# Optimization experiments

Hardware: AMD Instinct MI355X
Metric: run time of the kernel (lower is better)

Reference implementation:

```python
import jax, jax.numpy as jnp
import numpy as np

N_NODES = 50000
N_EDGES = 1600000
N_GRAPHS = 64
DIMS = [3, 256, 256, 256]  # in -> hidden -> hidden -> output
BN_EPS = 1e-5


def setup_inputs() -> dict:
    key = jax.random.key(0)
    ks = jax.random.split(key, 32)
    inp = {}
    inp['x'] = jax.random.normal(ks[0], (N_NODES, DIMS[0]), dtype=jnp.float32)
    inp['edge_index'] = jax.random.randint(ks[1], (2, N_EDGES), 0, N_NODES, dtype=jnp.int64)
    inp['batch'] = jnp.sort(jax.random.randint(ks[2], (N_NODES,), 0, N_GRAPHS, dtype=jnp.int64))
    k = 3
    for i in range(3):
        fi, fo = DIMS[i], DIMS[i + 1]
        inp[f'W{i}'] = jax.random.normal(ks[k], (fi, fo), dtype=jnp.float32) / np.sqrt(fi); k += 1
        inp[f'b{i}'] = jnp.zeros((fo,), dtype=jnp.float32)
        inp[f'g{i}'] = jnp.ones((fo,), dtype=jnp.float32)       # BN weight
        inp[f'be{i}'] = jnp.zeros((fo,), dtype=jnp.float32)     # BN bias
        inp[f'm{i}'] = 0.1 * jax.random.normal(ks[k], (fo,), dtype=jnp.float32); k += 1  # running mean
        inp[f'v{i}'] = jax.random.uniform(ks[k], (fo,), dtype=jnp.float32) + 0.5; k += 1  # running var
    return inp


def _gcn_norm(edge_index, n_nodes):
    # add self-loops, compute symmetric normalization (PyG GCNConv gcn_norm)
    loops = jnp.arange(n_nodes, dtype=edge_index.dtype)
    src = jnp.concatenate([edge_index[0], loops])
    dst = jnp.concatenate([edge_index[1], loops])
    deg = jax.ops.segment_sum(jnp.ones_like(dst, dtype=jnp.float32), dst, num_segments=n_nodes)
    dinv = jnp.where(deg > 0, jax.lax.rsqrt(deg), 0.0)
    norm = dinv[src] * dinv[dst]  # [E+N]
    return src, dst, norm


def _gcn_conv(x, W, b, src, dst, norm, n_nodes):
    h = x @ W                                 # [N, out]
    msg = h[src] * norm[:, None]              # gather + edge weight
    out = jax.ops.segment_sum(msg, dst, num_segments=n_nodes)  # scatter-add
    return out + b


def _bn_eval(x, g, be, m, v):
    return (x - m) * jax.lax.rsqrt(v + BN_EPS) * g + be


def _denan(x):
    return jnp.where(jnp.isnan(x), 0.0, x)


def reference(x, edge_index, batch,
              W0, b0, g0, be0, m0, v0,
              W1, b1, g1, be1, m1, v1,
              W2, b2, g2, be2, m2, v2):
    n = x.shape[0]
    src, dst, norm = _gcn_norm(edge_index, n)
    params = [(W0, b0, g0, be0, m0, v0), (W1, b1, g1, be1, m1, v1), (W2, b2, g2, be2, m2, v2)]
    h = x
    for i, (W, b, g, be, m, v) in enumerate(params):
        h = _gcn_conv(h, W, b, src, dst, norm, n)
        h = _bn_eval(h, g, be, m, v)
        if i < 2:
            h = jax.nn.relu(h)  # dropout is identity in eval mode
        h = _denan(h)
    # global_mean_pool over batch segments
    sums = jax.ops.segment_sum(h, batch, num_segments=N_GRAPHS)
    cnt = jax.ops.segment_sum(jnp.ones((n,), dtype=h.dtype), batch, num_segments=N_GRAPHS)
    out = sums / jnp.maximum(cnt, 1.0)[:, None]
    return _denan(out)
```

## Files before the change

kernel.cpp:

```cpp
#include <hip/hip_runtime.h>

#define NFEAT 256
#define BN_EPSF 1e-5f
#define CH_J 512
#define ELLW 96
#define BSH 7
#define PBKT 392
#define PCAP 4608
#define PEDG 4992

typedef __attribute__((ext_vector_type(8))) short bf16x8;
typedef __attribute__((ext_vector_type(4))) float f32x4;
typedef __attribute__((ext_vector_type(2))) float f32x2;

__device__ __forceinline__ unsigned short f2bf(float f) {
    union { float f; unsigned u; } v; v.f = f;
    unsigned r = v.u + 0x7fffu + ((v.u >> 16) & 1u);
    return (unsigned short)(r >> 16);
}
__device__ __forceinline__ float bf2f(unsigned short h) {
    union { unsigned u; float f; } v; v.u = ((unsigned)h) << 16;
    return v.f;
}


__global__ __launch_bounds__(256) void k_part(const int* __restrict__ src, const int* __restrict__ dst,
                                              int* __restrict__ curD, int* __restrict__ curS,
                                              unsigned* __restrict__ partD, unsigned* __restrict__ partS, int E) {
    __shared__ int cD[PBKT], cS[PBKT], bD[PBKT], bS[PBKT];
    __shared__ int2 eds[PEDG];
    for (int t = threadIdx.x; t < PBKT; t += 256) { cD[t] = 0; cS[t] = 0; }
    __syncthreads();
    int e0 = blockIdx.x * PEDG;
    int ne = min(E - e0, PEDG);
    for (int i = threadIdx.x; i < ne; i += 256) {
        int2 e; e.x = src[e0 + i]; e.y = dst[e0 + i];
        eds[i] = e;
        atomicAdd(&cD[e.y >> BSH], 1);
        atomicAdd(&cS[e.x >> BSH], 1);
    }
    __syncthreads();
    for (int t = threadIdx.x; t < PBKT; t += 256) {
        bD[t] = cD[t] ? atomicAdd(&curD[t], cD[t]) : 0;
        bS[t] = cS[t] ? atomicAdd(&curS[t], cS[t]) : 0;
        cD[t] = 0; cS[t] = 0;
    }
    __syncthreads();
    for (int i = threadIdx.x; i < ne; i += 256) {
        int2 e = eds[i];
        int b1 = e.y >> BSH;
        int p1 = bD[b1] + atomicAdd(&cD[b1], 1);
        if (p1 < PCAP) partD[(size_t)b1 * PCAP + p1] = ((unsigned)(e.y & 127) << 16) | (unsigned)e.x;
        int b2 = e.x >> BSH;
        int p2 = bS[b2] + atomicAdd(&cS[b2], 1);
        if (p2 < PCAP) partS[(size_t)b2 * PCAP + p2] = ((unsigned)(e.x & 127) << 16) | (unsigned)e.y;
    }
}

__global__ void k_xpack(const float* __restrict__ x, float4* __restrict__ x4, int N) {
    int i = blockIdx.x * blockDim.x + threadIdx.x;
    if (i < N) {
        float4 r; r.x = x[i * 3 + 0]; r.y = x[i * 3 + 1]; r.z = x[i * 3 + 2]; r.w = 0.f;
        x4[i] = r;
    }
}

__global__ __launch_bounds__(256) void k_buildIn(const unsigned* __restrict__ partD, const int* __restrict__ curD,
                                                 const int* __restrict__ batch,
                                                 unsigned short* __restrict__ ell_in, int* __restrict__ cnt,
                                                 float* __restrict__ dinv, float2* __restrict__ pack, int N) {
    __shared__ int rows[128][ELLW];
    __shared__ int cur[128];
    int b = blockIdx.x;
    if (threadIdx.x < 128) cur[threadIdx.x] = 0;
    __syncthreads();
    int lo = b << BSH;
    int ne = min(curD[b], PCAP);
    const unsigned* seg = partD + (size_t)b * PCAP;
    for (int i = threadIdx.x; i < ne; i += 256) {
        unsigned u = seg[i];
        int r = u >> 16;
        int pos = atomicAdd(&cur[r], 1);
        if (pos < ELLW) rows[r][pos] = (int)(u & 0xFFFFu);
    }
    __syncthreads();
    const int Q = ELLW / 8;
    for (int idx = threadIdx.x; idx < 128 * Q; idx += 256) {
        int r = idx / Q, q = idx % Q;
        if (lo + r < N) {
            unsigned short tmp[8];
#pragma unroll
            for (int j = 0; j < 8; j++) tmp[j] = (unsigned short)rows[r][q * 8 + j];
            *(uint4*)(ell_in + (size_t)(lo + r) * ELLW + q * 8) = *(const uint4*)tmp;
        }
    }
    if (threadIdx.x < 128) {
        int node = lo + threadIdx.x;
        if (node < N) {
            int c = cur[threadIdx.x];
            cnt[node] = c;
            float d = rsqrtf((float)(min(c, ELLW) + 1));
            dinv[node] = d;
            float2 pk; pk.x = d; pk.y = __int_as_float(batch[node]);
            pack[node] = pk;
        }
    }
}

__global__ __launch_bounds__(256) void k_buildCt(const unsigned* __restrict__ partS, const int* __restrict__ curS,
                                                 const float2* __restrict__ pack,
                                                 unsigned short* __restrict__ ct_hi,
                                                 unsigned short* __restrict__ ct_lo,
                                                 int N, int N_pad) {
    __shared__ float ct[128][65];
    __shared__ float dv[128];
    int b = blockIdx.x;
    for (int idx = threadIdx.x; idx < 128 * 65; idx += 256) (&ct[0][0])[idx] = 0.f;
    __syncthreads();
    int lo = b << BSH;
    int ne = min(curS[b], PCAP);
    const unsigned* seg = partS + (size_t)b * PCAP;
    for (int i = threadIdx.x; i < ne; i += 256) {
        unsigned u = seg[i];
        float2 pk = pack[u & 0xFFFFu];
        atomicAdd(&ct[u >> 16][__float_as_int(pk.y)], pk.x);
    }
    __syncthreads();
    if (threadIdx.x < 128) {
        int node = lo + threadIdx.x;
        if (node < N) {
            float2 ps = pack[node];
            dv[threadIdx.x] = ps.x;
            ct[threadIdx.x][__float_as_int(ps.y)] += ps.x;
        } else dv[threadIdx.x] = 0.f;
    }
    __syncthreads();
    int g = threadIdx.x >> 2, js = (threadIdx.x & 3) * 32;
    unsigned short hv[32], lv[32];
#pragma unroll
    for (int j = 0; j < 32; j++) {
        float val = dv[js + j] * ct[js + j][g];
        unsigned short h = f2bf(val);
        hv[j] = h;
        lv[j] = f2bf(val - bf2f(h));
    }
    size_t basep = (size_t)g * N_pad + lo + js;
#pragma unroll
    for (int j = 0; j < 32; j += 8) {
        *(uint4*)(ct_hi + basep + j) = *(const uint4*)&hv[j];
        *(uint4*)(ct_lo + basep + j) = *(const uint4*)&lv[j];
    }
}


__global__ __launch_bounds__(256) void k_wconv(const float* __restrict__ W, unsigned short* __restrict__ Wt) {
    int k = blockIdx.x, n = threadIdx.x;
    Wt[n * 256 + k] = f2bf(W[k * 256 + n]);
}


__global__ __launch_bounds__(256) void k_l0(const float4* __restrict__ x4, const unsigned short* __restrict__ ell_in,
                                            const int* __restrict__ cnt, const float* __restrict__ dinv,
                                            const float* __restrict__ W, const float* __restrict__ b,
                                            const float* __restrict__ g, const float* __restrict__ be,
                                            const float* __restrict__ m, const float* __restrict__ v,
                                            unsigned short* __restrict__ h, int N) {
    int wv = threadIdx.x >> 6, lane = threadIdx.x & 63;
    int node = blockIdx.x * 4 + wv;
    if (node >= N) return;
    float dvn = dinv[node];
    int len = min(cnt[node], ELLW);
    const unsigned short* nb = ell_in + (size_t)node * ELLW;
    float a0 = 0.f, a1 = 0.f, a2 = 0.f;
    for (int e = lane; e < len; e += 64) {
        int s = nb[e];
        float4 xv = x4[s];
        float w = dinv[s] * dvn;
        a0 += w * xv.x;
        a1 += w * xv.y;
        a2 += w * xv.z;
    }
#pragma unroll
    for (int off = 32; off; off >>= 1) {
        a0 += __shfl_xor(a0, off);
        a1 += __shfl_xor(a1, off);
        a2 += __shfl_xor(a2, off);
    }
    float4 xs = x4[node];
    float wself = dvn * dvn;
    a0 += wself * xs.x;
    a1 += wself * xs.y;
    a2 += wself * xs.z;
    int c4 = lane * 4;
    float4 w0 = *(const float4*)(W + c4);
    float4 w1 = *(const float4*)(W + NFEAT + c4);
    float4 w2 = *(const float4*)(W + 2 * NFEAT + c4);
    float4 bb = *(const float4*)(b + c4);
    float4 gg = *(const float4*)(g + c4);
    float4 ee = *(const float4*)(be + c4);
    float4 mm = *(const float4*)(m + c4);
    float4 vv = *(const float4*)(v + c4);
    float r0 = ((a0 * w0.x + a1 * w1.x + a2 * w2.x) + bb.x - mm.x) * rsqrtf(vv.x + BN_EPSF) * gg.x + ee.x;
    float r1 = ((a0 * w0.y + a1 * w1.y + a2 * w2.y) + bb.y - mm.y) * rsqrtf(vv.y + BN_EPSF) * gg.y + ee.y;
    float r2 = ((a0 * w0.z + a1 * w1.z + a2 * w2.z) + bb.z - mm.z) * rsqrtf(vv.z + BN_EPSF) * gg.z + ee.z;
    float r3 = ((a0 * w0.w + a1 * w1.w + a2 * w2.w) + bb.w - mm.w) * rsqrtf(vv.w + BN_EPSF) * gg.w + ee.w;
    ushort4 o;
    o.x = f2bf(fmaxf(r0, 0.f)); o.y = f2bf(fmaxf(r1, 0.f));
    o.z = f2bf(fmaxf(r2, 0.f)); o.w = f2bf(fmaxf(r3, 0.f));
    *(ushort4*)(h + (size_t)node * NFEAT + c4) = o;
}


__global__ __launch_bounds__(256) void k_mm_mfma(const unsigned short* __restrict__ A,
                                                 const unsigned short* __restrict__ Bt,
                                                 unsigned char* __restrict__ C8) {
    __shared__ __align__(16) unsigned short As[4][128][8];
    __shared__ __align__(16) unsigned short Bs[4][128][8];
    int bm = blockIdx.x * 128, bn = blockIdx.y * 128;
    int tid = threadIdx.x;
    int lane = tid & 63, wave = tid >> 6;
    int wm = (wave & 1) * 64, wn = (wave >> 1) * 64;
    int lrow = lane & 15, lk = lane >> 4;
    f32x4 acc[4][4] = {};

    for (int k0 = 0; k0 < 256; k0 += 32) {
#pragma unroll
        for (int i = 0; i < 2; i++) {
            int idx = tid + 256 * i;
            int ch = idx & 3, row = idx >> 2;
            *(uint4*)(&As[ch][row][0]) = *(const uint4*)(A + (size_t)(bm + row) * 256 + k0 + ch * 8);
            *(uint4*)(&Bs[ch][row][0]) = *(const uint4*)(Bt + (size_t)(bn + row) * 256 + k0 + ch * 8);
        }
        __syncthreads();
        bf16x8 af[4], bf[4];
#pragma unroll
        for (int r = 0; r < 4; r++) af[r] = *(const bf16x8*)(&As[lk][wm + r * 16 + lrow][0]);
#pragma unroll
        for (int c = 0; c < 4; c++) bf[c] = *(const bf16x8*)(&Bs[lk][wn + c * 16 + lrow][0]);
#pragma unroll
        for (int r = 0; r < 4; r++)
#pragma unroll
            for (int c = 0; c < 4; c++)
                acc[r][c] = __builtin_amdgcn_mfma_f32_16x16x32_bf16(af[r], bf[c], acc[r][c], 0, 0, 0);
        __syncthreads();
    }

#pragma unroll
    for (int r = 0; r < 4; r++) {
#pragma unroll
        for (int reg = 0; reg < 4; reg++) {
            int grow = bm + wm + r * 16 + lk * 4 + reg;
            int p01 = __builtin_amdgcn_cvt_pk_fp8_f32(acc[r][0][reg], acc[r][1][reg], 0, false);
            int p23 = __builtin_amdgcn_cvt_pk_fp8_f32(acc[r][2][reg], acc[r][3][reg], 0, false);
            size_t base = (size_t)grow * 256 + bn + wn + lrow;
            C8[base]      = (unsigned char)(p01 & 0xff);
            C8[base + 16] = (unsigned char)((p01 >> 8) & 0xff);
            C8[base + 32] = (unsigned char)(p23 & 0xff);
            C8[base + 48] = (unsigned char)((p23 >> 8) & 0xff);
        }
    }
}


template <bool RELU>
__global__ __launch_bounds__(64) void k_agg256b(const unsigned char* __restrict__ t,
                                                const unsigned short* __restrict__ ell_in,
                                                const int* __restrict__ cnt,
                                                const float* __restrict__ dinv,
                                                const float* __restrict__ b, const float* __restrict__ g,
                                                const float* __restrict__ be, const float* __restrict__ m,
                                                const float* __restrict__ v, unsigned short* __restrict__ out) {
    __shared__ int s_idx[64];
    __shared__ float s_w[64];
    int node = blockIdx.x;
    int c4 = threadIdx.x * 4;
    float dv = dinv[node];
    float a0, a1, a2, a3;
    {
        unsigned u = *(const unsigned*)(t + (size_t)node * NFEAT + c4);
        f32x2 flo = __builtin_amdgcn_cvt_pk_f32_fp8(u, false);
        f32x2 fhi = __builtin_amdgcn_cvt_pk_f32_fp8(u, true);
        float w = dv * dv;
        a0 = w * flo[0]; a1 = w * flo[1]; a2 = w * fhi[0]; a3 = w * fhi[1];
    }
    int len = min(cnt[node], ELLW);
    const unsigned short* nb = ell_in + (size_t)node * ELLW;
    for (int base = 0; base < len; base += 64) {
        int chunk = min(64, len - base);
        if ((int)threadIdx.x < chunk) {
            int s = nb[base + threadIdx.x];
            s_idx[threadIdx.x] = s;
            s_w[threadIdx.x] = dinv[s] * dv;
        }
        __syncthreads();
        int j = 0;
        for (; j + 4 <= chunk; j += 4) {
            unsigned u0 = *(const unsigned*)(t + (size_t)s_idx[j + 0] * NFEAT + c4);
            unsigned u1 = *(const unsigned*)(t + (size_t)s_idx[j + 1] * NFEAT + c4);
            unsigned u2 = *(const unsigned*)(t + (size_t)s_idx[j + 2] * NFEAT + c4);
            unsigned u3 = *(const unsigned*)(t + (size_t)s_idx[j + 3] * NFEAT + c4);
            float w0 = s_w[j + 0], w1 = s_w[j + 1], w2 = s_w[j + 2], w3 = s_w[j + 3];
            f32x2 l0 = __builtin_amdgcn_cvt_pk_f32_fp8(u0, false), h0 = __builtin_amdgcn_cvt_pk_f32_fp8(u0, true);
            f32x2 l1 = __builtin_amdgcn_cvt_pk_f32_fp8(u1, false), h1 = __builtin_amdgcn_cvt_pk_f32_fp8(u1, true);
            f32x2 l2 = __builtin_amdgcn_cvt_pk_f32_fp8(u2, false), h2 = __builtin_amdgcn_cvt_pk_f32_fp8(u2, true);
            f32x2 l3 = __builtin_amdgcn_cvt_pk_f32_fp8(u3, false), h3 = __builtin_amdgcn_cvt_pk_f32_fp8(u3, true);
            a0 += w0 * l0[0]; a1 += w0 * l0[1]; a2 += w0 * h0[0]; a3 += w0 * h0[1];
            a0 += w1 * l1[0]; a1 += w1 * l1[1]; a2 += w1 * h1[0]; a3 += w1 * h1[1];
            a0 += w2 * l2[0]; a1 += w2 * l2[1]; a2 += w2 * h2[0]; a3 += w2 * h2[1];
            a0 += w3 * l3[0]; a1 += w3 * l3[1]; a2 += w3 * h3[0]; a3 += w3 * h3[1];
        }
        for (; j < chunk; j++) {
            unsigned u = *(const unsigned*)(t + (size_t)s_idx[j] * NFEAT + c4);
            float w = s_w[j];
            f32x2 flo = __builtin_amdgcn_cvt_pk_f32_fp8(u, false);
            f32x2 fhi = __builtin_amdgcn_cvt_pk_f32_fp8(u, true);
            a0 += w * flo[0]; a1 += w * flo[1]; a2 += w * fhi[0]; a3 += w * fhi[1];
        }
        __syncthreads();
    }
    float4 bb = *(const float4*)(b + c4);
    float4 gg = *(const float4*)(g + c4);
    float4 ee = *(const float4*)(be + c4);
    float4 mm = *(const float4*)(m + c4);
    float4 vv = *(const float4*)(v + c4);
    float r0 = (a0 + bb.x - mm.x) * rsqrtf(vv.x + BN_EPSF) * gg.x + ee.x;
    float r1 = (a1 + bb.y - mm.y) * rsqrtf(vv.y + BN_EPSF) * gg.y + ee.y;
    float r2 = (a2 + bb.z - mm.z) * rsqrtf(vv.z + BN_EPSF) * gg.z + ee.z;
    float r3 = (a3 + bb.w - mm.w) * rsqrtf(vv.w + BN_EPSF) * gg.w + ee.w;
    if (RELU) { r0 = fmaxf(r0, 0.f); r1 = fmaxf(r1, 0.f); r2 = fmaxf(r2, 0.f); r3 = fmaxf(r3, 0.f); }
    ushort4 o; o.x = f2bf(r0); o.y = f2bf(r1); o.z = f2bf(r2); o.w = f2bf(r3);
    *(ushort4*)(out + (size_t)node * NFEAT + c4) = o;
}


__global__ __launch_bounds__(256) void k_cgemm(const unsigned short* __restrict__ Y,
                                               const unsigned short* __restrict__ ct_hi,
                                               const unsigned short* __restrict__ ct_lo,
                                               float* __restrict__ P, int N_pad) {
    __shared__ __align__(16) unsigned short s_hi[64 * 40];
    __shared__ __align__(16) unsigned short s_lo[64 * 40];
    int tid = threadIdx.x;
    int lane = tid & 63, wv = tid >> 6;
    int lc = lane & 15, q = lane >> 4;
    int cbase = blockIdx.y * 64 + wv * 16;
    int j0 = blockIdx.x * CH_J;
    int sg = tid >> 2, sj8 = (tid & 3) * 8;
    f32x4 acc[4] = {};

    for (int ks = 0; ks < CH_J; ks += 32) {
        size_t cbs = (size_t)sg * N_pad + j0 + ks + sj8;
        *(uint4*)(&s_hi[sg * 40 + sj8]) = *(const uint4*)(ct_hi + cbs);
        *(uint4*)(&s_lo[sg * 40 + sj8]) = *(const uint4*)(ct_lo + cbs);
        __syncthreads();
        const unsigned short* yp = Y + (size_t)(j0 + ks + q * 8) * 256 + cbase + lc;
        bf16x8 a;
#pragma unroll
        for (int jj = 0; jj < 8; jj++) a[jj] = (short)yp[(size_t)jj * 256];
#pragma unroll
        for (int nt = 0; nt < 4; nt++) {
            bf16x8 bh = *(const bf16x8*)(&s_hi[(nt * 16 + lc) * 40 + q * 8]);
            bf16x8 bl = *(const bf16x8*)(&s_lo[(nt * 16 + lc) * 40 + q * 8]);
            acc[nt] = __builtin_amdgcn_mfma_f32_16x16x32_bf16(a, bh, acc[nt], 0, 0, 0);
            acc[nt] = __builtin_amdgcn_mfma_f32_16x16x32_bf16(a, bl, acc[nt], 0, 0, 0);
        }
        __syncthreads();
    }
    float* pp = P + (size_t)blockIdx.x * 64 * 256;
#pragma unroll
    for (int nt = 0; nt < 4; nt++) {
        int g = nt * 16 + lc;
#pragma unroll
        for (int reg = 0; reg < 4; reg++) {
            int c = cbase + q * 4 + reg;
            pp[(size_t)c * 64 + g] = acc[nt][reg];
        }
    }
}

__global__ __launch_bounds__(64) void k_redP(const float* __restrict__ P,
                                             float* __restrict__ pooled, int nch) {
    int c = blockIdx.x;
    int g = threadIdx.x;
    float acc = 0.f;
    const float* pp = P + (size_t)c * 64 + g;
    for (int ch = 0; ch < nch; ch++) acc += pp[(size_t)ch * 64 * 256];
    pooled[(size_t)g * 256 + c] = acc;
}

__global__ __launch_bounds__(256) void k_out(const float* __restrict__ pooled,
                                             const float* __restrict__ W2,
                                             const int* __restrict__ batch,
                                             const float* __restrict__ b, const float* __restrict__ gw,
                                             const float* __restrict__ be, const float* __restrict__ m,
                                             const float* __restrict__ v,
                                             float* __restrict__ out, int N) {
    __shared__ float s_pool[256];
    __shared__ int s_cnt;
    int g = blockIdx.x;
    int c = threadIdx.x;
    s_pool[c] = pooled[(size_t)g * 256 + c];
    if (threadIdx.x == 0) {
        int lo = 0, hi = N;
        while (lo < hi) { int mid = (lo + hi) >> 1; if (batch[mid] < g) lo = mid + 1; else hi = mid; }
        int st = lo;
        lo = 0; hi = N;
        while (lo < hi) { int mid = (lo + hi) >> 1; if (batch[mid] < g + 1) lo = mid + 1; else hi = mid; }
        s_cnt = lo - st;
    }
    __syncthreads();
    float dot = 0.f;
    for (int k = 0; k < 256; k += 4) {
        float4 pk = *(const float4*)(s_pool + k);
        dot += pk.x * W2[(k + 0) * 256 + c];
        dot += pk.y * W2[(k + 1) * 256 + c];
        dot += pk.z * W2[(k + 2) * 256 + c];
        dot += pk.w * W2[(k + 3) * 256 + c];
    }
    float r = 0.f;
    int cntg = s_cnt;
    if (cntg > 0) {
        float mean = dot / (float)cntg + b[c];
        r = (mean - m[c]) * rsqrtf(v[c] + BN_EPSF) * gw[c] + be[c];
    }
    out[g * 256 + c] = r;
}


static inline size_t align_up(size_t x, size_t a) { return (x + a - 1) & ~(a - 1); }

extern "C" void kernel_launch(void* const* d_in, const int* in_sizes, int n_in,
                              void* d_out, int out_size, void* d_ws, size_t ws_size,
                              hipStream_t stream) {
    const float* x = (const float*)d_in[0];
    const int* edge_index = (const int*)d_in[1];
    const int* batch = (const int*)d_in[2];

    const int N = in_sizes[2];
    const int E = in_sizes[1] / 2;
    const int NCH = (N + CH_J - 1) / CH_J;
    const int N_pad = NCH * CH_J;

    const int* e_src = edge_index;
    const int* e_dst = edge_index + E;

    const float* W[3]; const float* bP[3]; const float* gP[3];
    const float* beP[3]; const float* mP[3]; const float* vP[3];
    for (int i = 0; i < 3; i++) {
        W[i]  = (const float*)d_in[3 + 6 * i + 0];
        bP[i] = (const float*)d_in[3 + 6 * i + 1];
        gP[i] = (const float*)d_in[3 + 6 * i + 2];
        beP[i]= (const float*)d_in[3 + 6 * i + 3];
        mP[i] = (const float*)d_in[3 + 6 * i + 4];
        vP[i] = (const float*)d_in[3 + 6 * i + 5];
    }

    char* ws = (char*)d_ws;
    size_t off = 0;
    auto carve = [&](size_t bytes) { void* p = ws + off; off = align_up(off + bytes, 256); return p; };
    int*   curD     = (int*)  carve((size_t)2 * PBKT * 4);
    int*   curS     = curD + PBKT;
    int*   cnt      = (int*)  carve((size_t)N * 4);
    float* dinv     = (float*)carve((size_t)N * 4);
    float2* pack    = (float2*)carve((size_t)N * 8);
    float4* x4      = (float4*)carve((size_t)N * 16);
    unsigned* partD = (unsigned*)carve((size_t)PBKT * PCAP * 4);
    unsigned* partS = (unsigned*)carve((size_t)PBKT * PCAP * 4);
    unsigned short* ell_in = (unsigned short*)carve((size_t)N * ELLW * 2);
    unsigned short* bufA = (unsigned short*)carve((size_t)N_pad * NFEAT * 2);
    unsigned char*  bufY = (unsigned char*)carve((size_t)N_pad * NFEAT);
    unsigned short* Wt1  = (unsigned short*)carve((size_t)NFEAT * NFEAT * 2);
    unsigned short* ct_hi = (unsigned short*)carve((size_t)N_pad * 64 * 2);
    unsigned short* ct_lo = (unsigned short*)carve((size_t)N_pad * 64 * 2);
    float* partials = (float*)carve((size_t)NCH * 64 * 256 * 4);
    float* pooled   = (float*)carve((size_t)64 * 256 * 4);
    (void)ws_size;

    hipMemsetAsync(curD, 0, (size_t)2 * PBKT * 4, stream);
    hipMemsetAsync(bufA + (size_t)N * NFEAT, 0, (size_t)(N_pad - N) * NFEAT * 2, stream);

    const int BS = 256;
    k_part<<<(E + PEDG - 1) / PEDG, BS, 0, stream>>>(e_src, e_dst, curD, curS, partD, partS, E);
    k_xpack<<<(N + BS - 1) / BS, BS, 0, stream>>>(x, x4, N);
    k_buildIn<<<PBKT, BS, 0, stream>>>(partD, curD, batch, ell_in, cnt, dinv, pack, N);
    k_buildCt<<<PBKT, BS, 0, stream>>>(partS, curS, pack, ct_hi, ct_lo, N, N_pad);
    k_wconv<<<NFEAT, NFEAT, 0, stream>>>(W[1], Wt1);

    k_l0<<<(N + 3) / 4, BS, 0, stream>>>(x4, ell_in, cnt, dinv, W[0],
                                         bP[0], gP[0], beP[0], mP[0], vP[0], bufA, N);

    dim3 mmGrid((N + 127) / 128, 2);
    k_mm_mfma<<<mmGrid, 256, 0, stream>>>(bufA, Wt1, bufY);
    k_agg256b<true><<<N, 64, 0, stream>>>(bufY, ell_in, cnt, dinv,
                                          bP[1], gP[1], beP[1], mP[1], vP[1], bufA);

    dim3 cgGrid(NCH, 4);
    k_cgemm<<<cgGrid, 256, 0, stream>>>(bufA, ct_hi, ct_lo, partials, N_pad);
    k_redP<<<256, 64, 0, stream>>>(partials, pooled, NCH);
    k_out<<<64, 256, 0, stream>>>(pooled, W[2], batch, bP[2], gP[2], beP[2], mP[2], vP[2],
                                  (float*)d_out, N);
}
```

Baseline: 332.6 us.

## Switch final pooling GEMM to FP8 MFMA with FP8 activations and scaled coefficients

The layer-1 aggregation output and the pooling coefficient matrix are now stored as FP8, with the coefficients split into hi/lo parts and scaled by 64, and the pooling GEMM uses fp8 MFMA instead of bf16. This halves the bytes read by the cgemm stage and in the coefficient build. It also merges the weight-conversion and x-packing kernels into one launch, replaces the padding memset with zero writes in padded blocks, and halves the chunk size for more cgemm parallelism. The main risk is accuracy, since layer-1 activations in FP8 lose a lot of precision.

```diff
diff --git a/kernel.cpp b/kernel.cpp
--- a/kernel.cpp
+++ b/kernel.cpp
@@ -2,12 +2,13 @@
 
 #define NFEAT 256
 #define BN_EPSF 1e-5f
-#define CH_J 512
+#define CH_J 256
 #define ELLW 96
 #define BSH 7
 #define PBKT 392
 #define PCAP 4608
 #define PEDG 4992
+#define CT_SCALE 64.0f
 
 typedef __attribute__((ext_vector_type(8))) short bf16x8;
 typedef __attribute__((ext_vector_type(4))) float f32x4;
@@ -57,11 +58,17 @@
     }
 }
 
-__global__ void k_xpack(const float* __restrict__ x, float4* __restrict__ x4, int N) {
-    int i = blockIdx.x * blockDim.x + threadIdx.x;
-    if (i < N) {
-        float4 r; r.x = x[i * 3 + 0]; r.y = x[i * 3 + 1]; r.z = x[i * 3 + 2]; r.w = 0.f;
-        x4[i] = r;
+__global__ __launch_bounds__(256) void k_prep(const float* __restrict__ W, unsigned short* __restrict__ Wt,
+                                              const float* __restrict__ x, float4* __restrict__ x4, int N) {
+    if (blockIdx.x < 256) {
+        int k = blockIdx.x, n = threadIdx.x;
+        Wt[n * 256 + k] = f2bf(W[k * 256 + n]);
+    } else {
+        int i = (blockIdx.x - 256) * 256 + threadIdx.x;
+        if (i < N) {
+            float4 r; r.x = x[i * 3 + 0]; r.y = x[i * 3 + 1]; r.z = x[i * 3 + 2]; r.w = 0.f;
+            x4[i] = r;
+        }
     }
 }
 
@@ -109,8 +116,8 @@
 
 __global__ __launch_bounds__(256) void k_buildCt(const unsigned* __restrict__ partS, const int* __restrict__ curS,
                                                  const float2* __restrict__ pack,
-                                                 unsigned short* __restrict__ ct_hi,
-                                                 unsigned short* __restrict__ ct_lo,
+                                                 unsigned char* __restrict__ ct_hi,
+                                                 unsigned char* __restrict__ ct_lo,
                                                  int N, int N_pad) {
     __shared__ float ct[128][65];
     __shared__ float dv[128];
@@ -136,26 +143,24 @@
     }
     __syncthreads();
     int g = threadIdx.x >> 2, js = (threadIdx.x & 3) * 32;
-    unsigned short hv[32], lv[32];
-#pragma unroll
-    for (int j = 0; j < 32; j++) {
-        float val = dv[js + j] * ct[js + j][g];
-        unsigned short h = f2bf(val);
-        hv[j] = h;
-        lv[j] = f2bf(val - bf2f(h));
+    unsigned char hv[32], lv[32];
+#pragma unroll
+    for (int p = 0; p < 16; p++) {
+        float v0 = dv[js + 2 * p] * ct[js + 2 * p][g] * CT_SCALE;
+        float v1 = dv[js + 2 * p + 1] * ct[js + 2 * p + 1][g] * CT_SCALE;
+        int ph = __builtin_amdgcn_cvt_pk_fp8_f32(v0, v1, 0, false);
+        f32x2 dec = __builtin_amdgcn_cvt_pk_f32_fp8(ph, false);
+        int pl = __builtin_amdgcn_cvt_pk_fp8_f32(v0 - dec[0], v1 - dec[1], 0, false);
+        hv[2 * p] = (unsigned char)(ph & 0xff);
+        hv[2 * p + 1] = (unsigned char)((ph >> 8) & 0xff);
+        lv[2 * p] = (unsigned char)(pl & 0xff);
+        lv[2 * p + 1] = (unsigned char)((pl >> 8) & 0xff);
     }
     size_t basep = (size_t)g * N_pad + lo + js;
-#pragma unroll
-    for (int j = 0; j < 32; j += 8) {
-        *(uint4*)(ct_hi + basep + j) = *(const uint4*)&hv[j];
-        *(uint4*)(ct_lo + basep + j) = *(const uint4*)&lv[j];
-    }
-}
-
-
-__global__ __launch_bounds__(256) void k_wconv(const float* __restrict__ W, unsigned short* __restrict__ Wt) {
-    int k = blockIdx.x, n = threadIdx.x;
-    Wt[n * 256 + k] = f2bf(W[k * 256 + n]);
+    *(uint4*)(ct_hi + basep) = *(const uint4*)&hv[0];
+    *(uint4*)(ct_hi + basep + 16) = *(const uint4*)&hv[16];
+    *(uint4*)(ct_lo + basep) = *(const uint4*)&lv[0];
+    *(uint4*)(ct_lo + basep + 16) = *(const uint4*)&lv[16];
 }
 
 
@@ -167,7 +172,12 @@
                                             unsigned short* __restrict__ h, int N) {
     int wv = threadIdx.x >> 6, lane = threadIdx.x & 63;
     int node = blockIdx.x * 4 + wv;
-    if (node >= N) return;
+    int c4 = lane * 4;
+    if (node >= N) {
+        ushort4 z = {0, 0, 0, 0};
+        *(ushort4*)(h + (size_t)node * NFEAT + c4) = z;
+        return;
+    }
     float dvn = dinv[node];
     int len = min(cnt[node], ELLW);
     const unsigned short* nb = ell_in + (size_t)node * ELLW;
@@ -191,7 +201,6 @@
     a0 += wself * xs.x;
     a1 += wself * xs.y;
     a2 += wself * xs.z;
-    int c4 = lane * 4;
     float4 w0 = *(const float4*)(W + c4);
     float4 w1 = *(const float4*)(W + NFEAT + c4);
     float4 w2 = *(const float4*)(W + 2 * NFEAT + c4);
@@ -269,11 +278,15 @@
                                                 const float* __restrict__ dinv,
                                                 const float* __restrict__ b, const float* __restrict__ g,
                                                 const float* __restrict__ be, const float* __restrict__ m,
-                                                const float* __restrict__ v, unsigned short* __restrict__ out) {
+                                                const float* __restrict__ v, unsigned char* __restrict__ out, int N) {
     __shared__ int s_idx[64];
     __shared__ float s_w[64];
     int node = blockIdx.x;
     int c4 = threadIdx.x * 4;
+    if (node >= N) {
+        *(unsigned*)(out + (size_t)node * NFEAT + c4) = 0u;
+        return;
+    }
     float dv = dinv[node];
     float a0, a1, a2, a3;
     {
@@ -328,17 +341,19 @@
     float r2 = (a2 + bb.z - mm.z) * rsqrtf(vv.z + BN_EPSF) * gg.z + ee.z;
     float r3 = (a3 + bb.w - mm.w) * rsqrtf(vv.w + BN_EPSF) * gg.w + ee.w;
     if (RELU) { r0 = fmaxf(r0, 0.f); r1 = fmaxf(r1, 0.f); r2 = fmaxf(r2, 0.f); r3 = fmaxf(r3, 0.f); }
-    ushort4 o; o.x = f2bf(r0); o.y = f2bf(r1); o.z = f2bf(r2); o.w = f2bf(r3);
-    *(ushort4*)(out + (size_t)node * NFEAT + c4) = o;
-}
-
-
-__global__ __launch_bounds__(256) void k_cgemm(const unsigned short* __restrict__ Y,
-                                               const unsigned short* __restrict__ ct_hi,
-                                               const unsigned short* __restrict__ ct_lo,
+    int p01 = __builtin_amdgcn_cvt_pk_fp8_f32(r0, r1, 0, false);
+    int p23 = __builtin_amdgcn_cvt_pk_fp8_f32(r2, r3, 0, false);
+    unsigned pk = (unsigned)(p01 & 0xffff) | ((unsigned)(p23 & 0xffff) << 16);
+    *(unsigned*)(out + (size_t)node * NFEAT + c4) = pk;
+}
+
+
+__global__ __launch_bounds__(256) void k_cgemm(const unsigned char* __restrict__ A1,
+                                               const unsigned char* __restrict__ ct_hi,
+                                               const unsigned char* __restrict__ ct_lo,
                                                float* __restrict__ P, int N_pad) {
-    __shared__ __align__(16) unsigned short s_hi[64 * 40];
-    __shared__ __align__(16) unsigned short s_lo[64 * 40];
+    __shared__ __align__(16) unsigned char s_hi[64 * 40];
+    __shared__ __align__(16) unsigned char s_lo[64 * 40];
     int tid = threadIdx.x;
     int lane = tid & 63, wv = tid >> 6;
     int lc = lane & 15, q = lane >> 4;
@@ -349,19 +364,19 @@
 
     for (int ks = 0; ks < CH_J; ks += 32) {
         size_t cbs = (size_t)sg * N_pad + j0 + ks + sj8;
-        *(uint4*)(&s_hi[sg * 40 + sj8]) = *(const uint4*)(ct_hi + cbs);
-        *(uint4*)(&s_lo[sg * 40 + sj8]) = *(const uint4*)(ct_lo + cbs);
+        *(uint2*)(&s_hi[sg * 40 + sj8]) = *(const uint2*)(ct_hi + cbs);
+        *(uint2*)(&s_lo[sg * 40 + sj8]) = *(const uint2*)(ct_lo + cbs);
         __syncthreads();
-        const unsigned short* yp = Y + (size_t)(j0 + ks + q * 8) * 256 + cbase + lc;
-        bf16x8 a;
-#pragma unroll
-        for (int jj = 0; jj < 8; jj++) a[jj] = (short)yp[(size_t)jj * 256];
+        const unsigned char* ap = A1 + (size_t)(j0 + ks + q * 8) * 256 + cbase + lc;
+        unsigned long long a = 0;
+#pragma unroll
+        for (int jj = 0; jj < 8; jj++) a |= (unsigned long long)ap[(size_t)jj * 256] << (8 * jj);
 #pragma unroll
         for (int nt = 0; nt < 4; nt++) {
-            bf16x8 bh = *(const bf16x8*)(&s_hi[(nt * 16 + lc) * 40 + q * 8]);
-            bf16x8 bl = *(const bf16x8*)(&s_lo[(nt * 16 + lc) * 40 + q * 8]);
-            acc[nt] = __builtin_amdgcn_mfma_f32_16x16x32_bf16(a, bh, acc[nt], 0, 0, 0);
-            acc[nt] = __builtin_amdgcn_mfma_f32_16x16x32_bf16(a, bl, acc[nt], 0, 0, 0);
+            unsigned long long bh = *(const unsigned long long*)(&s_hi[(nt * 16 + lc) * 40 + q * 8]);
+            unsigned long long bl = *(const unsigned long long*)(&s_lo[(nt * 16 + lc) * 40 + q * 8]);
+            acc[nt] = __builtin_amdgcn_mfma_f32_16x16x32_fp8_fp8((long)a, (long)bh, acc[nt], 0, 0, 0);
+            acc[nt] = __builtin_amdgcn_mfma_f32_16x16x32_fp8_fp8((long)a, (long)bl, acc[nt], 0, 0, 0);
         }
         __syncthreads();
     }
@@ -419,7 +434,7 @@
     float r = 0.f;
     int cntg = s_cnt;
     if (cntg > 0) {
-        float mean = dot / (float)cntg + b[c];
+        float mean = dot / (CT_SCALE * (float)cntg) + b[c];
         r = (mean - m[c]) * rsqrtf(v[c] + BN_EPSF) * gw[c] + be[c];
     }
     out[g * 256 + c] = r;
@@ -468,33 +483,32 @@
     unsigned short* ell_in = (unsigned short*)carve((size_t)N * ELLW * 2);
     unsigned short* bufA = (unsigned short*)carve((size_t)N_pad * NFEAT * 2);
     unsigned char*  bufY = (unsigned char*)carve((size_t)N_pad * NFEAT);
+    unsigned char*  bufA1 = (unsigned char*)carve((size_t)N_pad * NFEAT);
     unsigned short* Wt1  = (unsigned short*)carve((size_t)NFEAT * NFEAT * 2);
-    unsigned short* ct_hi = (unsigned short*)carve((size_t)N_pad * 64 * 2);
-    unsigned short* ct_lo = (unsigned short*)carve((size_t)N_pad * 64 * 2);
+    unsigned char*  ct_hi = (unsigned char*)carve((size_t)N_pad * 64);
+    unsigned char*  ct_lo = (unsigned char*)carve((size_t)N_pad * 64);
     float* partials = (float*)carve((size_t)NCH * 64 * 256 * 4);
     float* pooled   = (float*)carve((size_t)64 * 256 * 4);
     (void)ws_size;
 
     hipMemsetAsync(curD, 0, (size_t)2 * PBKT * 4, stream);
-    hipMemsetAsync(bufA + (size_t)N * NFEAT, 0, (size_t)(N_pad - N) * NFEAT * 2, stream);
 
     const int BS = 256;
     k_part<<<(E + PEDG - 1) / PEDG, BS, 0, stream>>>(e_src, e_dst, curD, curS, partD, partS, E);
-    k_xpack<<<(N + BS - 1) / BS, BS, 0, stream>>>(x, x4, N);
+    k_prep<<<256 + (N + BS - 1) / BS, BS, 0, stream>>>(W[1], Wt1, x, x4, N);
     k_buildIn<<<PBKT, BS, 0, stream>>>(partD, curD, batch, ell_in, cnt, dinv, pack, N);
     k_buildCt<<<PBKT, BS, 0, stream>>>(partS, curS, pack, ct_hi, ct_lo, N, N_pad);
-    k_wconv<<<NFEAT, NFEAT, 0, stream>>>(W[1], Wt1);
-
-    k_l0<<<(N + 3) / 4, BS, 0, stream>>>(x4, ell_in, cnt, dinv, W[0],
-                                         bP[0], gP[0], beP[0], mP[0], vP[0], bufA, N);
+
+    k_l0<<<N_pad / 4, BS, 0, stream>>>(x4, ell_in, cnt, dinv, W[0],
+                                       bP[0], gP[0], beP[0], mP[0], vP[0], bufA, N);
 
     dim3 mmGrid((N + 127) / 128, 2);
     k_mm_mfma<<<mmGrid, 256, 0, stream>>>(bufA, Wt1, bufY);
-    k_agg256b<true><<<N, 64, 0, stream>>>(bufY, ell_in, cnt, dinv,
-                                          bP[1], gP[1], beP[1], mP[1], vP[1], bufA);
+    k_agg256b<true><<<N_pad, 64, 0, stream>>>(bufY, ell_in, cnt, dinv,
+                                              bP[1], gP[1], beP[1], mP[1], vP[1], bufA1, N);
 
     dim3 cgGrid(NCH, 4);
-    k_cgemm<<<cgGrid, 256, 0, stream>>>(bufA, ct_hi, ct_lo, partials, N_pad);
+    k_cgemm<<<cgGrid, 256, 0, stream>>>(bufA1, ct_hi, ct_lo, partials, N_pad);
     k_redP<<<256, 64, 0, stream>>>(partials, pooled, NCH);
     k_out<<<64, 256, 0, stream>>>(pooled, W[2], batch, bP[2], gP[2], beP[2], mP[2], vP[2],
                                   (float*)d_out, N);
```

Result: slower. 344.5 us (+3.6%).
